# Performance work log

Measured on AMD Instinct MI355X. Metric: run time of the kernel, lower is better.

Reference implementation:

```python
import jax, jax.numpy as jnp
import numpy as np

B, L, DIN, H, E, K = 64, 256, 768, 64, 8, 2
S = 16  # sqrt(L): token<->feature grid side
LOSS_COEF = 1e-2


def gelu(x):
    return jax.nn.gelu(x, approximate=False)  # torch nn.GELU (exact erf)


def cv_squared(v):
    v = v.astype(jnp.float32)
    return jnp.var(v, ddof=1) / (jnp.mean(v) ** 2 + 1e-10)


def setup_inputs() -> dict:
    key = jax.random.key(0)
    ks = jax.random.split(key, 16)
    rn = lambda k, shape, s=0.02: jax.random.normal(k, shape, jnp.float32) * s
    lap = jnp.array([[0., 1., 0.], [1., -4., 1.], [0., 1., 0.]], jnp.float32)
    return {
        "x": jax.random.normal(ks[0], (B, L, DIN), jnp.float32),
        "dte": jax.random.normal(ks[1], (B, L, DIN), jnp.float32),
        "w_gate": rn(ks[2], (L, E), 1.0),
        "W_exp": rn(ks[3], (E, DIN, H)), "b_exp": jnp.zeros((E, H), jnp.float32),
        "W_sh": rn(ks[4], (DIN, H)), "b_sh": jnp.zeros((H,), jnp.float32),
        "ln_g": jnp.ones((H,), jnp.float32), "ln_b": jnp.zeros((H,), jnp.float32),
        "W_px": rn(ks[5], (H, 2 * H)), "b_px": jnp.zeros((2 * H,), jnp.float32),
        "conv_sh": jnp.tile(lap[None, None], (H, 1, 1, 1)),  # depthwise Laplacian [H,1,3,3]
        "W_pxx": rn(ks[6], (H, H)), "b_pxx": jnp.zeros((H,), jnp.float32),
        "W_dte": rn(ks[7], (H, H)), "b_dte": jnp.zeros((H,), jnp.float32),
        "W_dteall": rn(ks[8], (H, H)), "b_dteall": jnp.zeros((H,), jnp.float32),
        "W_rgb": rn(ks[9], (DIN, H)), "b_rgb": jnp.zeros((H,), jnp.float32),
        "W_fx": rn(ks[10], (H, H)), "b_fx": jnp.zeros((H,), jnp.float32),
        "W_fmod": rn(ks[11], (H, H)), "b_fmod": jnp.zeros((H,), jnp.float32),
        "W_fxx": rn(ks[12], (H, H)), "b_fxx": jnp.zeros((H,), jnp.float32),
    }


def reference(x, dte, w_gate, W_exp, b_exp, W_sh, b_sh, ln_g, ln_b, W_px, b_px,
              conv_sh, W_pxx, b_pxx, W_dte, b_dte, W_dteall, b_dteall,
              W_rgb, b_rgb, W_fx, b_fx, W_fmod, b_fmod, W_fxx, b_fxx):
    # ---- top-k gating (clean logits; noisy_gating=False / eval) ----
    logits = dte.mean(-1) @ w_gate                     # [B,E]
    topv, topi = jax.lax.top_k(logits, K)
    topg = jax.nn.softmax(topv, axis=1)
    gates = jnp.zeros_like(logits).at[jnp.arange(B)[:, None], topi].set(topg)
    importance = gates.sum(0)
    load = (gates > 0).sum(0).astype(jnp.float32)
    loss = LOSS_COEF * (cv_squared(importance) + cv_squared(load))
    # ---- sparse dispatch / expert Linear / weighted combine (dense-equivalent) ----
    y = jnp.einsum('be,bld,edh->blh', gates, dte, W_exp) + (gates @ b_exp)[:, None, :]
    # ---- shared expert Linear + Shared block ----
    sh = dte @ W_sh + b_sh                             # [B,L,H]
    shortcut = sh
    t = (sh - sh.mean(-1, keepdims=True)) * jax.lax.rsqrt(sh.var(-1, keepdims=True) + 1e-6)
    t = t * ln_g + ln_b
    t = t @ W_px + b_px                                # [B,L,2H]
    t1, t2 = t[..., :H], t[..., H:]
    f = t1.transpose(0, 2, 1).reshape(B, H, S, S)      # token2feature
    f = jax.lax.conv_general_dilated(f, conv_sh, (1, 1), 'SAME', feature_group_count=H)
    t1 = f.reshape(B, H, L).transpose(0, 2, 1)         # feature2token
    sh = (gelu(t1) * t2) @ W_pxx + b_pxx + shortcut
    # ---- combine MoE and shared streams ----
    dte_tok = (y @ W_dte + b_dte) + (sh @ W_dteall + b_dteall)
    rgb_tok = x @ W_rgb + b_rgb
    # ---- Fusion (its self.norm was overwritten to GELU; token<->feature round-trip is identity) ----
    shortcut = rgb_tok
    a = gelu(rgb_tok) @ W_fx + b_fx
    m = gelu(dte_tok) @ W_fmod + b_fmod
    out = (gelu(m) * a) @ W_fxx + b_fxx + shortcut     # [B,L,H]
    return out, loss
```

## Files before the change

### kernel.cpp

```cpp
#include <hip/hip_runtime.h>
#include <math.h>

typedef unsigned short u16;
typedef unsigned int u32;
typedef __attribute__((ext_vector_type(8))) short bf16x8;
typedef __attribute__((ext_vector_type(4))) float f32x4;


__device__ __forceinline__ float bf2f(u16 u) {
    union { u32 i; float f; } x; x.i = ((u32)u) << 16; return x.f;
}
__device__ __forceinline__ u16 f2bf(float f) {
    union { float f; u32 i; } x; x.f = f;
    u32 i = x.i;
    return (u16)((i + 0x7fffu + ((i >> 16) & 1u)) >> 16);
}
__device__ __forceinline__ u32 pack2(float a, float b) {
    return (u32)f2bf(a) | ((u32)f2bf(b) << 16);
}
__device__ __forceinline__ float wsum(float v) {
    #pragma unroll
    for (int o = 1; o < 64; o <<= 1) v += __shfl_xor(v, o, 64);
    return v;
}
__device__ __forceinline__ float gelu_f(float x) {
    return 0.5f * x * (1.0f + erff(x * 0.70710678118654752440f));
}

__global__ __launch_bounds__(256) void k_gate_part(const float* __restrict__ dte,
                                                   const float* __restrict__ w_gate,
                                                   float* __restrict__ partial) {
    __shared__ float dmeanS[64];
    int p = blockIdx.x, tid = threadIdx.x, w = tid >> 6, lane = tid & 63;
    for (int i = 0; i < 16; i++) {
        int l = w * 16 + i;
        const float* pr = dte + ((size_t)p * 64 + l) * 768;
        float s = 0.f;
        #pragma unroll
        for (int j = 0; j < 3; j++) {
            float4 v = *(const float4*)(pr + (lane + j * 64) * 4);
            s += v.x + v.y + v.z + v.w;
        }
        s = wsum(s);
        if (lane == 0) dmeanS[l] = s * (1.f / 768.f);
    }
    __syncthreads();
    if (w == 0) {
        float dm = dmeanS[lane];
        int wl = (p & 3) * 64 + lane;
        #pragma unroll
        for (int e = 0; e < 8; e++) {
            float s = wsum(dm * w_gate[wl * 8 + e]);
            if (lane == 0) partial[p * 8 + e] = s;
        }
    }
}

__global__ __launch_bounds__(256) void k_gate_fin(const float* __restrict__ partial,
                                                  const float* __restrict__ b_exp,
                                                  int* __restrict__ topi,
                                                  float* __restrict__ topg,
                                                  float* __restrict__ bias_y,
                                                  float* __restrict__ loss_out) {
    __shared__ float gS[64 * 8];
    __shared__ int i0S[64], i1S[64];
    __shared__ float g0S[64], g1S[64];
    int tid = threadIdx.x;
    if (tid < 64) {
        float lg[8];
        #pragma unroll
        for (int e = 0; e < 8; e++)
            lg[e] = partial[(tid * 4 + 0) * 8 + e] + partial[(tid * 4 + 1) * 8 + e] +
                    partial[(tid * 4 + 2) * 8 + e] + partial[(tid * 4 + 3) * 8 + e];
        int i0 = 0; float v0 = lg[0];
        #pragma unroll
        for (int e = 1; e < 8; e++) if (lg[e] > v0) { v0 = lg[e]; i0 = e; }
        int i1 = -1; float v1 = -1e30f;
        #pragma unroll
        for (int e = 0; e < 8; e++) if (e != i0 && lg[e] > v1) { v1 = lg[e]; i1 = e; }
        if (i1 < 0) i1 = (i0 + 1) & 7;
        float e2 = expf(v1 - v0);
        float g0 = 1.f / (1.f + e2);
        float g1 = e2 / (1.f + e2);
        #pragma unroll
        for (int e = 0; e < 8; e++) gS[tid * 8 + e] = 0.f;
        gS[tid * 8 + i0] = g0;
        gS[tid * 8 + i1] = g1;
        i0S[tid] = i0; i1S[tid] = i1; g0S[tid] = g0; g1S[tid] = g1;
        topi[tid * 2] = i0; topi[tid * 2 + 1] = i1;
        topg[tid * 2] = g0; topg[tid * 2 + 1] = g1;
    }
    __syncthreads();
    for (int idx = tid; idx < 4096; idx += 256) {
        int b = idx >> 6, h = idx & 63;
        bias_y[idx] = g0S[b] * b_exp[i0S[b] * 64 + h] + g1S[b] * b_exp[i1S[b] * 64 + h];
    }
    if (tid < 64) {
        float g[8];
        #pragma unroll
        for (int e = 0; e < 8; e++) g[e] = gS[tid * 8 + e];
        float imp[8], ld[8];
        #pragma unroll
        for (int e = 0; e < 8; e++) {
            imp[e] = wsum(g[e]);
            ld[e]  = wsum(g[e] > 0.f ? 1.f : 0.f);
        }
        if (tid == 0) {
            float l = 0.f;
            {
                float s = 0.f;
                #pragma unroll
                for (int e = 0; e < 8; e++) s += imp[e];
                float mn = s / 8.f, v = 0.f;
                #pragma unroll
                for (int e = 0; e < 8; e++) { float d = imp[e] - mn; v += d * d; }
                l += (v / 7.f) / (mn * mn + 1e-10f);
            }
            {
                float s = 0.f;
                #pragma unroll
                for (int e = 0; e < 8; e++) s += ld[e];
                float mn = s / 8.f, v = 0.f;
                #pragma unroll
                for (int e = 0; e < 8; e++) { float d = ld[e] - mn; v += d * d; }
                l += (v / 7.f) / (mn * mn + 1e-10f);
            }
            loss_out[0] = 0.01f * l;
        }
    }
}

__global__ __launch_bounds__(256) void k_gemm3(const float* __restrict__ dte,
                                               const float* __restrict__ x,
                                               const float* __restrict__ W_sh,
                                               const float* __restrict__ b_sh,
                                               const float* __restrict__ W_exp,
                                               const int* __restrict__ topi,
                                               const float* __restrict__ topg,
                                               const float* __restrict__ bias_y,
                                               const float* __restrict__ W_rgb,
                                               const float* __restrict__ b_rgb,
                                               float* __restrict__ buf_sh,
                                               u16* __restrict__ buf_y,
                                               float* __restrict__ out_rgb) {
    __shared__ u16 As[64 * 72];
    __shared__ u16 Wt[64 * 72];
    int bid = blockIdx.x;
    int kind, row0;
    if (bid < 512) { kind = bid & 1; row0 = (bid >> 1) * 64; }
    else           { kind = 2;       row0 = (bid - 512) * 64; }
    int b = row0 >> 8;
    int tid = threadIdx.x, wv = tid >> 6, lane = tid & 63;
    int m = lane & 15, quad = lane >> 4;

    const float* A = (kind == 2) ? x : dte;
    const float* W0 = (kind == 2) ? W_rgb : W_sh;
    const float* W1 = W0;
    float g0 = 0.f, g1 = 0.f;
    if (kind == 1) {
        W0 = W_exp + (size_t)topi[2 * b] * 49152;
        W1 = W_exp + (size_t)topi[2 * b + 1] * 49152;
        g0 = topg[2 * b]; g1 = topg[2 * b + 1];
    }

    float4 pa[2][2];
    float  pw[16];
    const int a_r  = tid >> 3;
    const int a_k8 = (tid & 7) * 8;
    const int w_n  = tid & 63;
    const int w_k0 = (tid >> 6) * 16;

    auto loadA = [&](int kc) {
        #pragma unroll
        for (int j = 0; j < 2; j++) {
            const float* src = A + (size_t)(row0 + a_r + j * 32) * 768 + kc * 64 + a_k8;
            pa[j][0] = *(const float4*)(src);
            pa[j][1] = *(const float4*)(src + 4);
        }
    };
    auto loadW = [&](int kc) {
        if (kind == 1) {
            #pragma unroll
            for (int j = 0; j < 16; j++) {
                size_t off = (size_t)(kc * 64 + w_k0 + j) * 64 + w_n;
                pw[j] = g0 * W0[off] + g1 * W1[off];
            }
        } else {
            #pragma unroll
            for (int j = 0; j < 16; j++)
                pw[j] = W0[(size_t)(kc * 64 + w_k0 + j) * 64 + w_n];
        }
    };
    auto stageLDS = [&]() {
        #pragma unroll
        for (int j = 0; j < 2; j++) {
            uint4 d;
            d.x = pack2(pa[j][0].x, pa[j][0].y);
            d.y = pack2(pa[j][0].z, pa[j][0].w);
            d.z = pack2(pa[j][1].x, pa[j][1].y);
            d.w = pack2(pa[j][1].z, pa[j][1].w);
            *(uint4*)&As[(a_r + j * 32) * 72 + a_k8] = d;
        }
        uint4 d0, d1;
        d0.x = pack2(pw[0],  pw[1]);  d0.y = pack2(pw[2],  pw[3]);
        d0.z = pack2(pw[4],  pw[5]);  d0.w = pack2(pw[6],  pw[7]);
        d1.x = pack2(pw[8],  pw[9]);  d1.y = pack2(pw[10], pw[11]);
        d1.z = pack2(pw[12], pw[13]); d1.w = pack2(pw[14], pw[15]);
        *(uint4*)&Wt[w_n * 72 + w_k0]     = d0;
        *(uint4*)&Wt[w_n * 72 + w_k0 + 8] = d1;
    };

    f32x4 acc0 = {0.f, 0.f, 0.f, 0.f}, acc1 = acc0, acc2 = acc0, acc3 = acc0;

    loadA(0); loadW(0);
    for (int kc = 0; kc < 12; kc++) {
        __syncthreads();
        stageLDS();
        __syncthreads();
        if (kc < 11) { loadA(kc + 1); loadW(kc + 1); }
        const int ar = (wv * 16 + m) * 72;
        bf16x8 a0 = *(const bf16x8*)&As[ar + quad * 8];
        bf16x8 a1 = *(const bf16x8*)&As[ar + 32 + quad * 8];
        #pragma unroll
        for (int t = 0; t < 4; t++) {
            const int br = (t * 16 + m) * 72;
            bf16x8 b0 = *(const bf16x8*)&Wt[br + quad * 8];
            bf16x8 b1 = *(const bf16x8*)&Wt[br + 32 + quad * 8];
            f32x4* accp = (t == 0) ? &acc0 : (t == 1) ? &acc1 : (t == 2) ? &acc2 : &acc3;
            *accp = __builtin_amdgcn_mfma_f32_16x16x32_bf16(a0, b0, *accp, 0, 0, 0);
            *accp = __builtin_amdgcn_mfma_f32_16x16x32_bf16(a1, b1, *accp, 0, 0, 0);
        }
    }

    f32x4 accs[4] = {acc0, acc1, acc2, acc3};
    #pragma unroll
    for (int t = 0; t < 4; t++) {
        int col = t * 16 + m;
        float bias;
        if (kind == 0)      bias = b_sh[col];
        else if (kind == 1) bias = bias_y[b * 64 + col];
        else                bias = b_rgb[col];
        #pragma unroll
        for (int i = 0; i < 4; i++) {
            int r = row0 + wv * 16 + quad * 4 + i;
            float val = accs[t][i] + bias;
            if (kind == 0)      buf_sh[(size_t)r * 64 + col] = val;
            else if (kind == 1) buf_y[(size_t)r * 64 + col] = f2bf(val);
            else                out_rgb[(size_t)r * 64 + col] = val;
        }
    }
}

__global__ __launch_bounds__(256) void k_lnpx(const float* __restrict__ buf_sh,
                                              const float* __restrict__ ln_g,
                                              const float* __restrict__ ln_b,
                                              const float* __restrict__ W_px,
                                              const float* __restrict__ b_px,
                                              u16* __restrict__ t1, u16* __restrict__ t2) {
    __shared__ float T[32 * 68];
    __shared__ float Wpx[8192];
    int r0 = blockIdx.x * 32;
    int tid = threadIdx.x, w = tid >> 6, lane = tid & 63;
    #pragma unroll
    for (int j = 0; j < 8; j++) {
        int e4 = tid + j * 256;
        *(float4*)(Wpx + e4 * 4) = *(const float4*)(W_px + e4 * 4);
    }
    float lnG = ln_g[lane], lnB = ln_b[lane];
    for (int i = 0; i < 8; i++) {
        int l = w * 8 + i;
        float v = buf_sh[(size_t)(r0 + l) * 64 + lane];
        float mean = wsum(v) * (1.f / 64.f);
        float d = v - mean;
        float var = wsum(d * d) * (1.f / 64.f);
        T[l * 68 + lane] = d * rsqrtf(var + 1e-6f) * lnG + lnB;
    }
    __syncthreads();
    int rg = tid >> 4, cg = tid & 15;
    float acc1[2][4] = {}, acc2[2][4] = {};
    const float* tr = T + rg * 2 * 68;
    #pragma unroll 4
    for (int kk = 0; kk < 64; kk++) {
        float a0 = tr[kk], a1 = tr[68 + kk];
        float4 w1 = *(const float4*)(Wpx + kk * 128 + cg * 4);
        float4 w2 = *(const float4*)(Wpx + kk * 128 + 64 + cg * 4);
        acc1[0][0] += a0 * w1.x; acc1[0][1] += a0 * w1.y; acc1[0][2] += a0 * w1.z; acc1[0][3] += a0 * w1.w;
        acc1[1][0] += a1 * w1.x; acc1[1][1] += a1 * w1.y; acc1[1][2] += a1 * w1.z; acc1[1][3] += a1 * w1.w;
        acc2[0][0] += a0 * w2.x; acc2[0][1] += a0 * w2.y; acc2[0][2] += a0 * w2.z; acc2[0][3] += a0 * w2.w;
        acc2[1][0] += a1 * w2.x; acc2[1][1] += a1 * w2.y; acc2[1][2] += a1 * w2.z; acc2[1][3] += a1 * w2.w;
    }
    float4 b1 = *(const float4*)(b_px + cg * 4);
    float4 b2 = *(const float4*)(b_px + 64 + cg * 4);
    #pragma unroll
    for (int i = 0; i < 2; i++) {
        int r = r0 + rg * 2 + i;
        u32* d1 = (u32*)(t1 + (size_t)r * 64 + cg * 4);
        d1[0] = pack2(acc1[i][0] + b1.x, acc1[i][1] + b1.y);
        d1[1] = pack2(acc1[i][2] + b1.z, acc1[i][3] + b1.w);
        u32* d2 = (u32*)(t2 + (size_t)r * 64 + cg * 4);
        d2[0] = pack2(acc2[i][0] + b2.x, acc2[i][1] + b2.y);
        d2[1] = pack2(acc2[i][2] + b2.z, acc2[i][3] + b2.w);
    }
}

__global__ __launch_bounds__(256) void k_tail(const u16* __restrict__ t1,
                                              const u16* __restrict__ t2,
                                              const float* __restrict__ conv_sh,
                                              const float* __restrict__ W_pxx,
                                              const float* __restrict__ b_pxx,
                                              const float* __restrict__ buf_sh,
                                              const u16* __restrict__ buf_y,
                                              const float* __restrict__ W_dte,
                                              const float* __restrict__ b_dte,
                                              const float* __restrict__ W_dteall,
                                              const float* __restrict__ b_dteall,
                                              const float* __restrict__ W_fx,
                                              const float* __restrict__ b_fx,
                                              const float* __restrict__ W_fmod,
                                              const float* __restrict__ b_fmod,
                                              const float* __restrict__ W_fxx,
                                              const float* __restrict__ b_fxx,
                                              float* __restrict__ out) {
    __shared__ float C0[32 * 68];
    __shared__ float GA[32 * 68];
    __shared__ float SH1[32 * 68];
    __shared__ float GM[32 * 68];
    __shared__ u16   Ybh[32 * 72];
    __shared__ __align__(16) float WL[2][4096];
    int r0 = blockIdx.x * 32;
    int tid = threadIdx.x, w = tid >> 6, lane = tid & 63;
    int rg = tid >> 4, cg = tid & 15;

    auto stage_w = [&](const float* __restrict__ Wsrc, int half) {
        const float* g = Wsrc + w * 1024 + lane * 4;
        float* l = &WL[half][w * 1024];
        #pragma unroll
        for (int j = 0; j < 4; j++) {
            __builtin_amdgcn_global_load_lds(
                (const __attribute__((address_space(1))) unsigned int*)(g + j * 256),
                (__attribute__((address_space(3))) unsigned int*)(l + j * 256),
                16, 0, 0);
        }
    };

    stage_w(W_pxx, 0);

    stage_w(W_dte, 1);
    float4 rsv[2];
    #pragma unroll
    for (int i = 0; i < 2; i++) {
        int r = rg * 2 + i;
        uint2 v = *(const uint2*)(buf_y + (size_t)(r0 + r) * 64 + cg * 4);
        *(uint2*)(&Ybh[r * 72 + cg * 4]) = v;
        rsv[i] = *(const float4*)(out + (size_t)(r0 + r) * 64 + cg * 4);
        GA[r * 68 + cg * 4 + 0] = gelu_f(rsv[i].x);
        GA[r * 68 + cg * 4 + 1] = gelu_f(rsv[i].y);
        GA[r * 68 + cg * 4 + 2] = gelu_f(rsv[i].z);
        GA[r * 68 + cg * 4 + 3] = gelu_f(rsv[i].w);
    }
    {
        float c0 = conv_sh[lane * 9 + 0], c1 = conv_sh[lane * 9 + 1], c2 = conv_sh[lane * 9 + 2];
        float c3 = conv_sh[lane * 9 + 3], c4 = conv_sh[lane * 9 + 4], c5 = conv_sh[lane * 9 + 5];
        float c6 = conv_sh[lane * 9 + 6], c7 = conv_sh[lane * 9 + 7], c8 = conv_sh[lane * 9 + 8];
        #pragma unroll
        for (int i = 0; i < 8; i++) {
            int l = w * 8 + i;
            int gr = r0 + l;
            int pix = gr & 255, ii = pix >> 4, jj = pix & 15;
            const u16* p = t1 + (size_t)gr * 64 + lane;
            float c = c4 * bf2f(p[0]);
            if (ii > 0) {
                c += c1 * bf2f(p[-1024]);
                if (jj > 0)  c += c0 * bf2f(p[-1024 - 64]);
                if (jj < 15) c += c2 * bf2f(p[-1024 + 64]);
            }
            if (jj > 0)  c += c3 * bf2f(p[-64]);
            if (jj < 15) c += c5 * bf2f(p[64]);
            if (ii < 15) {
                c += c7 * bf2f(p[1024]);
                if (jj > 0)  c += c6 * bf2f(p[1024 - 64]);
                if (jj < 15) c += c8 * bf2f(p[1024 + 64]);
            }
            C0[l * 68 + lane] = gelu_f(c) * bf2f(t2[(size_t)gr * 64 + lane]);
        }
    }
    __syncthreads();

    {
        float acc[2][4] = {};
        const float* ur = C0 + rg * 2 * 68;
        #pragma unroll 8
        for (int kk = 0; kk < 64; kk++) {
            float a0 = ur[kk], a1 = ur[68 + kk];
            float4 wv = *(const float4*)(&WL[0][kk * 64 + cg * 4]);
            acc[0][0] += a0 * wv.x; acc[0][1] += a0 * wv.y; acc[0][2] += a0 * wv.z; acc[0][3] += a0 * wv.w;
            acc[1][0] += a1 * wv.x; acc[1][1] += a1 * wv.y; acc[1][2] += a1 * wv.z; acc[1][3] += a1 * wv.w;
        }
        float4 bp = *(const float4*)(b_pxx + cg * 4);
        #pragma unroll
        for (int i = 0; i < 2; i++) {
            int r = rg * 2 + i;
            float4 shv = *(const float4*)(buf_sh + (size_t)(r0 + r) * 64 + cg * 4);
            *(float4*)(SH1 + r * 68 + cg * 4) =
                make_float4(acc[i][0] + bp.x + shv.x, acc[i][1] + bp.y + shv.y,
                            acc[i][2] + bp.z + shv.z, acc[i][3] + bp.w + shv.w);
        }
    }
    __syncthreads();

    float accC[2][4] = {};
    stage_w(W_dteall, 0);
    {
        const u16* yr = Ybh + rg * 2 * 72;
        #pragma unroll 8
        for (int kk = 0; kk < 64; kk++) {
            float y0 = bf2f(yr[kk]), y1 = bf2f(yr[72 + kk]);
            float4 wv = *(const float4*)(&WL[1][kk * 64 + cg * 4]);
            accC[0][0] += y0 * wv.x; accC[0][1] += y0 * wv.y; accC[0][2] += y0 * wv.z; accC[0][3] += y0 * wv.w;
            accC[1][0] += y1 * wv.x; accC[1][1] += y1 * wv.y; accC[1][2] += y1 * wv.z; accC[1][3] += y1 * wv.w;
        }
    }
    __syncthreads();

    stage_w(W_fx, 1);
    {
        const float* sr = SH1 + rg * 2 * 68;
        #pragma unroll 8
        for (int kk = 0; kk < 64; kk++) {
            float s0 = sr[kk], s1 = sr[68 + kk];
            float4 wv = *(const float4*)(&WL[0][kk * 64 + cg * 4]);
            accC[0][0] += s0 * wv.x; accC[0][1] += s0 * wv.y; accC[0][2] += s0 * wv.z; accC[0][3] += s0 * wv.w;
            accC[1][0] += s1 * wv.x; accC[1][1] += s1 * wv.y; accC[1][2] += s1 * wv.z; accC[1][3] += s1 * wv.w;
        }
        float4 bd1 = *(const float4*)(b_dte + cg * 4);
        float4 bd2 = *(const float4*)(b_dteall + cg * 4);
        #pragma unroll
        for (int i = 0; i < 2; i++) {
            int r = rg * 2 + i;
            *(float4*)(GM + r * 68 + cg * 4) =
                make_float4(gelu_f(accC[i][0] + bd1.x + bd2.x), gelu_f(accC[i][1] + bd1.y + bd2.y),
                            gelu_f(accC[i][2] + bd1.z + bd2.z), gelu_f(accC[i][3] + bd1.w + bd2.w));
        }
    }
    __syncthreads();

    float accA[2][4] = {};
    stage_w(W_fmod, 0);
    {
        const float* ga = GA + rg * 2 * 68;
        #pragma unroll 8
        for (int kk = 0; kk < 64; kk++) {
            float a0 = ga[kk], a1 = ga[68 + kk];
            float4 wv = *(const float4*)(&WL[1][kk * 64 + cg * 4]);
            accA[0][0] += a0 * wv.x; accA[0][1] += a0 * wv.y; accA[0][2] += a0 * wv.z; accA[0][3] += a0 * wv.w;
            accA[1][0] += a1 * wv.x; accA[1][1] += a1 * wv.y; accA[1][2] += a1 * wv.z; accA[1][3] += a1 * wv.w;
        }
    }
    __syncthreads();

    stage_w(W_fxx, 1);
    {
        float accM[2][4] = {};
        const float* gm = GM + rg * 2 * 68;
        #pragma unroll 8
        for (int kk = 0; kk < 64; kk++) {
            float m0 = gm[kk], m1 = gm[68 + kk];
            float4 wv = *(const float4*)(&WL[0][kk * 64 + cg * 4]);
            accM[0][0] += m0 * wv.x; accM[0][1] += m0 * wv.y; accM[0][2] += m0 * wv.z; accM[0][3] += m0 * wv.w;
            accM[1][0] += m1 * wv.x; accM[1][1] += m1 * wv.y; accM[1][2] += m1 * wv.z; accM[1][3] += m1 * wv.w;
        }
        float4 bx = *(const float4*)(b_fx + cg * 4);
        float4 bm = *(const float4*)(b_fmod + cg * 4);
        #pragma unroll
        for (int i = 0; i < 2; i++) {
            int r = rg * 2 + i;
            float a0 = accA[i][0] + bx.x, a1 = accA[i][1] + bx.y, a2 = accA[i][2] + bx.z, a3 = accA[i][3] + bx.w;
            float m0 = accM[i][0] + bm.x, m1 = accM[i][1] + bm.y, m2 = accM[i][2] + bm.z, m3 = accM[i][3] + bm.w;
            *(float4*)(C0 + r * 68 + cg * 4) =
                make_float4(gelu_f(m0) * a0, gelu_f(m1) * a1, gelu_f(m2) * a2, gelu_f(m3) * a3);
        }
    }
    __syncthreads();

    {
        float acc[2][4] = {};
        const float* pr = C0 + rg * 2 * 68;
        #pragma unroll 8
        for (int kk = 0; kk < 64; kk++) {
            float p0 = pr[kk], p1 = pr[68 + kk];
            float4 wv = *(const float4*)(&WL[1][kk * 64 + cg * 4]);
            acc[0][0] += p0 * wv.x; acc[0][1] += p0 * wv.y; acc[0][2] += p0 * wv.z; acc[0][3] += p0 * wv.w;
            acc[1][0] += p1 * wv.x; acc[1][1] += p1 * wv.y; acc[1][2] += p1 * wv.z; acc[1][3] += p1 * wv.w;
        }
        float4 bo = *(const float4*)(b_fxx + cg * 4);
        #pragma unroll
        for (int i = 0; i < 2; i++) {
            int r = rg * 2 + i;
            *(float4*)(out + (size_t)(r0 + r) * 64 + cg * 4) =
                make_float4(acc[i][0] + bo.x + rsv[i].x, acc[i][1] + bo.y + rsv[i].y,
                            acc[i][2] + bo.z + rsv[i].z, acc[i][3] + bo.w + rsv[i].w);
        }
    }
}

extern "C" void kernel_launch(void* const* d_in, const int* in_sizes, int n_in,
                              void* d_out, int out_size, void* d_ws, size_t ws_size,
                              hipStream_t stream) {
    const float* x       = (const float*)d_in[0];
    const float* dte     = (const float*)d_in[1];
    const float* w_gate  = (const float*)d_in[2];
    const float* W_exp   = (const float*)d_in[3];
    const float* b_exp   = (const float*)d_in[4];
    const float* W_sh    = (const float*)d_in[5];
    const float* b_sh    = (const float*)d_in[6];
    const float* ln_g    = (const float*)d_in[7];
    const float* ln_b    = (const float*)d_in[8];
    const float* W_px    = (const float*)d_in[9];
    const float* b_px    = (const float*)d_in[10];
    const float* conv_sh = (const float*)d_in[11];
    const float* W_pxx   = (const float*)d_in[12];
    const float* b_pxx   = (const float*)d_in[13];
    const float* W_dte   = (const float*)d_in[14];
    const float* b_dte   = (const float*)d_in[15];
    const float* W_dteall= (const float*)d_in[16];
    const float* b_dteall= (const float*)d_in[17];
    const float* W_rgb   = (const float*)d_in[18];
    const float* b_rgb   = (const float*)d_in[19];
    const float* W_fx    = (const float*)d_in[20];
    const float* b_fx    = (const float*)d_in[21];
    const float* W_fmod  = (const float*)d_in[22];
    const float* b_fmod  = (const float*)d_in[23];
    const float* W_fxx   = (const float*)d_in[24];
    const float* b_fxx   = (const float*)d_in[25];

    float* out = (float*)d_out;

    float* wsf    = (float*)d_ws;
    float* partial= wsf;
    int*   topi   = (int*)(wsf + 2048);
    float* topg   = wsf + 2176;
    float* bias_y = wsf + 2304;
    float* buf_sh = wsf + 8192;
    u16*   buf_y  = (u16*)(wsf + 8192 + 1048576);
    u16*   t1     = (u16*)(wsf + 8192 + 1048576 + 524288);
    u16*   t2     = (u16*)(wsf + 8192 + 1048576 + 524288*2);

    hipLaunchKernelGGL(k_gate_part, dim3(256), dim3(256), 0, stream, dte, w_gate, partial);
    hipLaunchKernelGGL(k_gate_fin, dim3(1), dim3(256), 0, stream,
                       partial, b_exp, topi, topg, bias_y, out + 1048576);
    hipLaunchKernelGGL(k_gemm3, dim3(768), dim3(256), 0, stream,
                       dte, x, W_sh, b_sh, W_exp, topi, topg, bias_y, W_rgb, b_rgb,
                       buf_sh, buf_y, out);
    hipLaunchKernelGGL(k_lnpx, dim3(512), dim3(256), 0, stream,
                       buf_sh, ln_g, ln_b, W_px, b_px, t1, t2);
    hipLaunchKernelGGL(k_tail, dim3(512), dim3(256), 0, stream,
                       t1, t2, conv_sh, W_pxx, b_pxx, buf_sh, buf_y,
                       W_dte, b_dte, W_dteall, b_dteall,
                       W_fx, b_fx, W_fmod, b_fmod, W_fxx, b_fxx, out);

    (void)in_sizes; (void)n_in; (void)out_size; (void)ws_size;
}
```

Measured before the change: 242.2 us.

## Fuse shared and expert GEMMs over dte, batch gate loads, use LDS DMA

The shared-expert and routed-expert GEMMs both read the same dte tile, so they now run in one block that stages the A tile once and keeps two weight tiles and two accumulator sets. This halves the dte reads for those GEMMs and cuts the grid from 768 to 512 blocks. The gate-mean kernel now issues eight rows of loads before reducing, to raise memory-level parallelism. bf16 conversion now uses the HIP intrinsics, and the W_px staging in k_lnpx uses global_load_lds direct-to-LDS loads. The costs are more registers and LDS per block in the fused GEMM, and load imbalance between fused and rgb-only blocks. The global_load_lds path is followed by no explicit wait beyond the existing syncthreads, which carries a correctness risk.

```diff
diff --git a/kernel.cpp b/kernel.cpp
--- a/kernel.cpp
+++ b/kernel.cpp
@@ -1,4 +1,5 @@
 #include <hip/hip_runtime.h>
+#include <hip/hip_bf16.h>
 #include <math.h>
 
 typedef unsigned short u16;
@@ -11,12 +12,14 @@
     union { u32 i; float f; } x; x.i = ((u32)u) << 16; return x.f;
 }
 __device__ __forceinline__ u16 f2bf(float f) {
-    union { float f; u32 i; } x; x.f = f;
-    u32 i = x.i;
-    return (u16)((i + 0x7fffu + ((i >> 16) & 1u)) >> 16);
+    union { __hip_bfloat16 h; u16 u; } x;
+    x.h = __float2bfloat16(f);
+    return x.u;
 }
 __device__ __forceinline__ u32 pack2(float a, float b) {
-    return (u32)f2bf(a) | ((u32)f2bf(b) << 16);
+    union { __hip_bfloat162 h; u32 u; } x;
+    x.h = __float22bfloat162_rn(make_float2(a, b));
+    return x.u;
 }
 __device__ __forceinline__ float wsum(float v) {
     #pragma unroll
@@ -32,17 +35,25 @@
                                                    float* __restrict__ partial) {
     __shared__ float dmeanS[64];
     int p = blockIdx.x, tid = threadIdx.x, w = tid >> 6, lane = tid & 63;
-    for (int i = 0; i < 16; i++) {
-        int l = w * 16 + i;
-        const float* pr = dte + ((size_t)p * 64 + l) * 768;
-        float s = 0.f;
-        #pragma unroll
-        for (int j = 0; j < 3; j++) {
-            float4 v = *(const float4*)(pr + (lane + j * 64) * 4);
-            s += v.x + v.y + v.z + v.w;
-        }
-        s = wsum(s);
-        if (lane == 0) dmeanS[l] = s * (1.f / 768.f);
+    #pragma unroll
+    for (int h = 0; h < 2; h++) {
+        float4 v[8][3];
+        #pragma unroll
+        for (int i = 0; i < 8; i++) {
+            const float* pr = dte + ((size_t)p * 64 + w * 16 + h * 8 + i) * 768;
+            #pragma unroll
+            for (int j = 0; j < 3; j++)
+                v[i][j] = *(const float4*)(pr + (lane + j * 64) * 4);
+        }
+        #pragma unroll
+        for (int i = 0; i < 8; i++) {
+            float s = 0.f;
+            #pragma unroll
+            for (int j = 0; j < 3; j++)
+                s += v[i][j].x + v[i][j].y + v[i][j].z + v[i][j].w;
+            s = wsum(s);
+            if (lane == 0) dmeanS[w * 16 + h * 8 + i] = s * (1.f / 768.f);
+        }
     }
     __syncthreads();
     if (w == 0) {
@@ -143,28 +154,30 @@
                                                float* __restrict__ buf_sh,
                                                u16* __restrict__ buf_y,
                                                float* __restrict__ out_rgb) {
-    __shared__ u16 As[64 * 72];
-    __shared__ u16 Wt[64 * 72];
+    __shared__ __align__(16) u16 As[64 * 72];
+    __shared__ __align__(16) u16 Wt0[64 * 72];
+    __shared__ __align__(16) u16 Wt1[64 * 72];
     int bid = blockIdx.x;
-    int kind, row0;
-    if (bid < 512) { kind = bid & 1; row0 = (bid >> 1) * 64; }
-    else           { kind = 2;       row0 = (bid - 512) * 64; }
+    bool fused = bid < 256;
+    int row0 = fused ? bid * 64 : (bid - 256) * 64;
     int b = row0 >> 8;
     int tid = threadIdx.x, wv = tid >> 6, lane = tid & 63;
     int m = lane & 15, quad = lane >> 4;
 
-    const float* A = (kind == 2) ? x : dte;
-    const float* W0 = (kind == 2) ? W_rgb : W_sh;
-    const float* W1 = W0;
+    const float* A  = fused ? dte : x;
+    const float* Wb = fused ? W_sh : W_rgb;
+    const float* We0 = W_exp;
+    const float* We1 = W_exp;
     float g0 = 0.f, g1 = 0.f;
-    if (kind == 1) {
-        W0 = W_exp + (size_t)topi[2 * b] * 49152;
-        W1 = W_exp + (size_t)topi[2 * b + 1] * 49152;
+    if (fused) {
+        We0 = W_exp + (size_t)topi[2 * b] * 49152;
+        We1 = W_exp + (size_t)topi[2 * b + 1] * 49152;
         g0 = topg[2 * b]; g1 = topg[2 * b + 1];
     }
 
     float4 pa[2][2];
-    float  pw[16];
+    float  pw0[16];
+    float  pw1[16];
     const int a_r  = tid >> 3;
     const int a_k8 = (tid & 7) * 8;
     const int w_n  = tid & 63;
@@ -179,16 +192,15 @@
         }
     };
     auto loadW = [&](int kc) {
-        if (kind == 1) {
+        #pragma unroll
+        for (int j = 0; j < 16; j++)
+            pw0[j] = Wb[(size_t)(kc * 64 + w_k0 + j) * 64 + w_n];
+        if (fused) {
             #pragma unroll
             for (int j = 0; j < 16; j++) {
                 size_t off = (size_t)(kc * 64 + w_k0 + j) * 64 + w_n;
-                pw[j] = g0 * W0[off] + g1 * W1[off];
-            }
-        } else {
-            #pragma unroll
-            for (int j = 0; j < 16; j++)
-                pw[j] = W0[(size_t)(kc * 64 + w_k0 + j) * 64 + w_n];
+                pw1[j] = g0 * We0[off] + g1 * We1[off];
+            }
         }
     };
     auto stageLDS = [&]() {
@@ -201,16 +213,29 @@
             d.w = pack2(pa[j][1].z, pa[j][1].w);
             *(uint4*)&As[(a_r + j * 32) * 72 + a_k8] = d;
         }
-        uint4 d0, d1;
-        d0.x = pack2(pw[0],  pw[1]);  d0.y = pack2(pw[2],  pw[3]);
-        d0.z = pack2(pw[4],  pw[5]);  d0.w = pack2(pw[6],  pw[7]);
-        d1.x = pack2(pw[8],  pw[9]);  d1.y = pack2(pw[10], pw[11]);
-        d1.z = pack2(pw[12], pw[13]); d1.w = pack2(pw[14], pw[15]);
-        *(uint4*)&Wt[w_n * 72 + w_k0]     = d0;
-        *(uint4*)&Wt[w_n * 72 + w_k0 + 8] = d1;
+        {
+            uint4 d0, d1;
+            d0.x = pack2(pw0[0],  pw0[1]);  d0.y = pack2(pw0[2],  pw0[3]);
+            d0.z = pack2(pw0[4],  pw0[5]);  d0.w = pack2(pw0[6],  pw0[7]);
+            d1.x = pack2(pw0[8],  pw0[9]);  d1.y = pack2(pw0[10], pw0[11]);
+            d1.z = pack2(pw0[12], pw0[13]); d1.w = pack2(pw0[14], pw0[15]);
+            *(uint4*)&Wt0[w_n * 72 + w_k0]     = d0;
+            *(uint4*)&Wt0[w_n * 72 + w_k0 + 8] = d1;
+        }
+        if (fused) {
+            uint4 d0, d1;
+            d0.x = pack2(pw1[0],  pw1[1]);  d0.y = pack2(pw1[2],  pw1[3]);
+            d0.z = pack2(pw1[4],  pw1[5]);  d0.w = pack2(pw1[6],  pw1[7]);
+            d1.x = pack2(pw1[8],  pw1[9]);  d1.y = pack2(pw1[10], pw1[11]);
+            d1.z = pack2(pw1[12], pw1[13]); d1.w = pack2(pw1[14], pw1[15]);
+            *(uint4*)&Wt1[w_n * 72 + w_k0]     = d0;
+            *(uint4*)&Wt1[w_n * 72 + w_k0 + 8] = d1;
+        }
     };
 
-    f32x4 acc0 = {0.f, 0.f, 0.f, 0.f}, acc1 = acc0, acc2 = acc0, acc3 = acc0;
+    f32x4 z = {0.f, 0.f, 0.f, 0.f};
+    f32x4 s0 = z, s1 = z, s2 = z, s3 = z;
+    f32x4 y0 = z, y1 = z, y2 = z, y3 = z;
 
     loadA(0); loadW(0);
     for (int kc = 0; kc < 12; kc++) {
@@ -224,29 +249,42 @@
         #pragma unroll
         for (int t = 0; t < 4; t++) {
             const int br = (t * 16 + m) * 72;
-            bf16x8 b0 = *(const bf16x8*)&Wt[br + quad * 8];
-            bf16x8 b1 = *(const bf16x8*)&Wt[br + 32 + quad * 8];
-            f32x4* accp = (t == 0) ? &acc0 : (t == 1) ? &acc1 : (t == 2) ? &acc2 : &acc3;
-            *accp = __builtin_amdgcn_mfma_f32_16x16x32_bf16(a0, b0, *accp, 0, 0, 0);
-            *accp = __builtin_amdgcn_mfma_f32_16x16x32_bf16(a1, b1, *accp, 0, 0, 0);
-        }
-    }
-
-    f32x4 accs[4] = {acc0, acc1, acc2, acc3};
+            bf16x8 b0 = *(const bf16x8*)&Wt0[br + quad * 8];
+            bf16x8 b1 = *(const bf16x8*)&Wt0[br + 32 + quad * 8];
+            f32x4* sp = (t == 0) ? &s0 : (t == 1) ? &s1 : (t == 2) ? &s2 : &s3;
+            *sp = __builtin_amdgcn_mfma_f32_16x16x32_bf16(a0, b0, *sp, 0, 0, 0);
+            *sp = __builtin_amdgcn_mfma_f32_16x16x32_bf16(a1, b1, *sp, 0, 0, 0);
+            if (fused) {
+                bf16x8 c0 = *(const bf16x8*)&Wt1[br + quad * 8];
+                bf16x8 c1 = *(const bf16x8*)&Wt1[br + 32 + quad * 8];
+                f32x4* yp = (t == 0) ? &y0 : (t == 1) ? &y1 : (t == 2) ? &y2 : &y3;
+                *yp = __builtin_amdgcn_mfma_f32_16x16x32_bf16(a0, c0, *yp, 0, 0, 0);
+                *yp = __builtin_amdgcn_mfma_f32_16x16x32_bf16(a1, c1, *yp, 0, 0, 0);
+            }
+        }
+    }
+
+    f32x4 accs0[4] = {s0, s1, s2, s3};
+    f32x4 accs1[4] = {y0, y1, y2, y3};
     #pragma unroll
     for (int t = 0; t < 4; t++) {
         int col = t * 16 + m;
-        float bias;
-        if (kind == 0)      bias = b_sh[col];
-        else if (kind == 1) bias = bias_y[b * 64 + col];
-        else                bias = b_rgb[col];
-        #pragma unroll
-        for (int i = 0; i < 4; i++) {
-            int r = row0 + wv * 16 + quad * 4 + i;
-            float val = accs[t][i] + bias;
-            if (kind == 0)      buf_sh[(size_t)r * 64 + col] = val;
-            else if (kind == 1) buf_y[(size_t)r * 64 + col] = f2bf(val);
-            else                out_rgb[(size_t)r * 64 + col] = val;
+        if (fused) {
+            float bs = b_sh[col];
+            float by = bias_y[b * 64 + col];
+            #pragma unroll
+            for (int i = 0; i < 4; i++) {
+                int r = row0 + wv * 16 + quad * 4 + i;
+                buf_sh[(size_t)r * 64 + col] = accs0[t][i] + bs;
+                buf_y[(size_t)r * 64 + col]  = f2bf(accs1[t][i] + by);
+            }
+        } else {
+            float br = b_rgb[col];
+            #pragma unroll
+            for (int i = 0; i < 4; i++) {
+                int r = row0 + wv * 16 + quad * 4 + i;
+                out_rgb[(size_t)r * 64 + col] = accs0[t][i] + br;
+            }
         }
     }
 }
@@ -258,13 +296,17 @@
                                               const float* __restrict__ b_px,
                                               u16* __restrict__ t1, u16* __restrict__ t2) {
     __shared__ float T[32 * 68];
-    __shared__ float Wpx[8192];
+    __shared__ __align__(16) float Wpx[8192];
     int r0 = blockIdx.x * 32;
     int tid = threadIdx.x, w = tid >> 6, lane = tid & 63;
     #pragma unroll
     for (int j = 0; j < 8; j++) {
-        int e4 = tid + j * 256;
-        *(float4*)(Wpx + e4 * 4) = *(const float4*)(W_px + e4 * 4);
+        const float* g = W_px + (size_t)(w * 64 + j * 256) * 4 + lane * 4;
+        float* l = Wpx + (w * 64 + j * 256) * 4;
+        __builtin_amdgcn_global_load_lds(
+            (const __attribute__((address_space(1))) unsigned int*)g,
+            (__attribute__((address_space(3))) unsigned int*)l,
+            16, 0, 0);
     }
     float lnG = ln_g[lane], lnB = ln_b[lane];
     for (int i = 0; i < 8; i++) {
@@ -548,7 +590,7 @@
     hipLaunchKernelGGL(k_gate_part, dim3(256), dim3(256), 0, stream, dte, w_gate, partial);
     hipLaunchKernelGGL(k_gate_fin, dim3(1), dim3(256), 0, stream,
                        partial, b_exp, topi, topg, bias_y, out + 1048576);
-    hipLaunchKernelGGL(k_gemm3, dim3(768), dim3(256), 0, stream,
+    hipLaunchKernelGGL(k_gemm3, dim3(512), dim3(256), 0, stream,
                        dte, x, W_sh, b_sh, W_exp, topi, topg, bias_y, W_rgb, b_rgb,
                        buf_sh, buf_y, out);
     hipLaunchKernelGGL(k_lnpx, dim3(512), dim3(256), 0, stream,
```

Result: faster. 235.7 us (-2.7%).
